# Optimization experiments

Hardware: AMD Instinct MI355X
Metric: run time of the kernel (lower is better)

Reference implementation:

```python
import jax, jax.numpy as jnp
import numpy as np

H = 2048
W = 2048

# 2x2 derivative kernels (classic Lucas-Kanade / Horn-Schunck estimates)
_KX = np.array([[-1.0, 1.0], [-1.0, 1.0]], dtype=np.float32) * 0.25
_KY = np.array([[-1.0, -1.0], [1.0, 1.0]], dtype=np.float32) * 0.25
_KT = np.array([[1.0, 1.0], [1.0, 1.0]], dtype=np.float32) * 0.25


def _conv2d(x, k, padding):
    # x: (H, W), k: (kh, kw) -> (H', W')
    return jax.lax.conv_general_dilated(
        x[None, None], k[None, None].astype(x.dtype), (1, 1), padding
    )[0, 0]


def _deriv(img, k):
    # replicate-pad bottom/right so the 2x2 valid conv returns (H, W)
    p = jnp.pad(img, ((0, 1), (0, 1)), mode='edge')
    return _conv2d(p, jnp.asarray(k), 'VALID')


def setup_inputs() -> dict:
    key = jax.random.key(0)
    k1, k2 = jax.random.split(key)
    image_prev = jax.random.uniform(k1, (1, 1, H, W), dtype=jnp.float32)
    image_next = jax.random.uniform(k2, (1, 1, H, W), dtype=jnp.float32)
    return {"image_prev": image_prev, "image_next": image_next, "window_size": 15}


def reference(image_prev, image_next, window_size):
    prev = image_prev[0, 0]  # (H, W); original code only uses batch 0, channel 0
    nxt = image_next[0, 0]

    fx = 0.5 * (_deriv(prev, _KX) + _deriv(nxt, _KX))
    fy = 0.5 * (_deriv(prev, _KY) + _deriv(nxt, _KY))
    ft = _deriv(nxt, _KT) - _deriv(prev, _KT)

    w = int(window_size)
    ones = jnp.ones((w, w), dtype=fx.dtype)

    def box(f):
        # window sum with zero padding == ZeroPad2d(n) + w x w sliding sum
        return _conv2d(f, ones, 'SAME')

    Axx = box(fx * fx)
    Axy = box(fx * fy)
    Ayy = box(fy * fy)
    bx = box(fx * ft)
    by = box(fy * ft)

    det = Axx * Ayy - Axy * Axy
    valid = det != 0
    safe_det = jnp.where(valid, det, jnp.ones_like(det))
    # [[Axx,Axy],[Axy,Ayy]]^{-1} @ [bx, by]
    u = jnp.where(valid, (Ayy * bx - Axy * by) / safe_det, 0.0)
    v = jnp.where(valid, (Axx * by - Axy * bx) / safe_det, 0.0)

    return jnp.stack([u, v])[None]  # (1, 2, H, W)
```

## Files before the change

kernel.cpp:

```cpp
#include <hip/hip_runtime.h>


constexpr int IH  = 2048;
constexpr int IW  = 2048;
constexpr int RAD = 7;
constexpr int WIN = 15;
constexpr int NT  = 256;
constexpr int SW  = 112;
constexpr int RB  = 4;
constexpr int SCAN = RB + WIN - 1;
constexpr int NSTRIP = 19;
constexpr int NBAND  = IH / RB;
constexpr int NGRP   = NBAND / 4;
constexpr int NXCD   = 8;
constexpr int CHUNK  = NGRP / NXCD;

struct Row { float sp0, sp1, dt0, dt1; };

template<bool YE>
__device__ __forceinline__ Row load_row(const float* __restrict__ P,
                                        const float* __restrict__ N,
                                        int row, int pcb, bool lload) {
    if constexpr (YE) row = row < 0 ? 0 : (row > IH - 1 ? IH - 1 : row);
    float2 q = make_float2(0.f, 0.f), r = q;
    if (lload) {
        const size_t off = (size_t)row * IW + pcb;
        q = *reinterpret_cast<const float2*>(P + off);
        r = *reinterpret_cast<const float2*>(N + off);
    }
    Row R;
    R.sp0 = q.x + r.x; R.dt0 = r.x - q.x;
    R.sp1 = q.y + r.y; R.dt1 = r.y - q.y;
    return R;
}

template<bool SUB, bool XE>
__device__ __forceinline__ void accum(float V[5][2], const Row& A, const Row& B,
                                      int t, bool ok, bool rep2) {
    const float g0 = A.sp0 + B.sp0, g1 = A.sp1 + B.sp1;
    const float m0 = B.sp0 - A.sp0, m1 = B.sp1 - A.sp1;
    const float e0 = A.dt0 + B.dt0, e1 = A.dt1 + B.dt1;
    float g2 = __shfl(g0, t + 1);
    float m2 = __shfl(m0, t + 1);
    float e2 = __shfl(e0, t + 1);
    if constexpr (XE) {
        g2 = rep2 ? g1 : g2; m2 = rep2 ? m1 : m2; e2 = rep2 ? e1 : e2;
    }
    float fx0 = g1 - g0, fy0 = m0 + m1, ft0 = e0 + e1;
    float fx1 = g2 - g1, fy1 = m1 + m2, ft1 = e1 + e2;
    if constexpr (XE) {
        fx0 = ok ? fx0 : 0.f; fy0 = ok ? fy0 : 0.f; ft0 = ok ? ft0 : 0.f;
        fx1 = ok ? fx1 : 0.f; fy1 = ok ? fy1 : 0.f; ft1 = ok ? ft1 : 0.f;
    }
    if constexpr (!SUB) {
        V[0][0] += fx0 * fx0; V[1][0] += fx0 * fy0; V[2][0] += fy0 * fy0;
        V[3][0] += fx0 * ft0; V[4][0] += fy0 * ft0;
        V[0][1] += fx1 * fx1; V[1][1] += fx1 * fy1; V[2][1] += fy1 * fy1;
        V[3][1] += fx1 * ft1; V[4][1] += fy1 * ft1;
    } else {
        V[0][0] -= fx0 * fx0; V[1][0] -= fx0 * fy0; V[2][0] -= fy0 * fy0;
        V[3][0] -= fx0 * ft0; V[4][0] -= fy0 * ft0;
        V[0][1] -= fx1 * fx1; V[1][1] -= fx1 * fy1; V[2][1] -= fy1 * fy1;
        V[3][1] -= fx1 * ft1; V[4][1] -= fy1 * ft1;
    }
}

template<bool XE, bool YE>
__device__ __forceinline__ void lk_body(const float* __restrict__ P,
                                        const float* __restrict__ N,
                                        float* __restrict__ out,
                                        int c0, int r0, int t) {
    const int pcb = c0 - 8 + 2 * t;
    bool ok = true, rep2 = false;
    if constexpr (XE) {
        ok   = ((unsigned)pcb < (unsigned)IW);
        rep2 = (pcb + 2 >= IW) && ok;
    }
    const bool lload = ok;

    float V[5][2] = {};

    Row E0 = load_row<YE>(P, N, r0 - 7, pcb, lload);
    Row E1 = load_row<YE>(P, N, r0 - 6, pcb, lload);
    Row E2 = load_row<YE>(P, N, r0 - 5, pcb, lload);
    Row X0 = E0, X1 = E1, X2 = E2, X3;

    #pragma unroll
    for (int sr = 0; sr < SCAN; ++sr) {
        const int pr = r0 - RAD + sr;

        Row nE;
        const bool doE = (sr <= 15);
        if (doE) nE = load_row<YE>(P, N, pr + 3, pcb, lload);

        bool enter_ok = true;
        if constexpr (YE) enter_ok = (pr >= 0) && (pr < IH);
        if (enter_ok) accum<false, XE>(V, E0, E1, t, ok, rep2);

        if (sr >= 15) {
            bool exit_ok = true;
            if constexpr (YE) exit_ok = (pr - WIN) >= 0;
            if (exit_ok) {
                if (sr == 15) accum<true, XE>(V, X0, X1, t, ok, rep2);
                if (sr == 16) accum<true, XE>(V, X1, X2, t, ok, rep2);
                if (sr == 17) accum<true, XE>(V, X2, X3, t, ok, rep2);
            }
        }

        if (sr >= WIN - 1) {
            float a0[5], a1[5];
            #pragma unroll
            for (int p = 0; p < 5; ++p) {
                const float Pg = V[p][0] + V[p][1];
                float S = Pg + __shfl(Pg, t + 1);
                S += __shfl(S, t + 2);
                S += __shfl(S, t + 4);
                const float q0 = __shfl(V[p][0], t + 8);
                a0[p] = S - V[p][0];
                a1[p] = (S - Pg) + q0;
            }
            const float det0 = a0[0] * a0[2] - a0[1] * a0[1];
            const float rd0  = __builtin_amdgcn_rcpf(det0) * 2.0f;
            const bool  k0   = (det0 != 0.f);
            const float det1 = a1[0] * a1[2] - a1[1] * a1[1];
            const float rd1  = __builtin_amdgcn_rcpf(det1) * 2.0f;
            const bool  k1   = (det1 != 0.f);
            float2 qu, qv;
            qu.x = k0 ? (a0[2] * a0[3] - a0[1] * a0[4]) * rd0 : 0.f;
            qv.x = k0 ? (a0[0] * a0[4] - a0[1] * a0[3]) * rd0 : 0.f;
            qu.y = k1 ? (a1[2] * a1[3] - a1[1] * a1[4]) * rd1 : 0.f;
            qv.y = k1 ? (a1[0] * a1[4] - a1[1] * a1[3]) * rd1 : 0.f;

            const int i  = r0 + sr - (WIN - 1);
            const int x0 = c0 + 2 * t;
            const bool st = (2 * t < SW) && (x0 < IW);
            if (st) {
                *reinterpret_cast<float2*>(out + (size_t)i * IW + x0) = qu;
                *reinterpret_cast<float2*>(out + (size_t)IH * IW + (size_t)i * IW + x0) = qv;
            }
        }

        E0 = E1; E1 = E2; if (doE) E2 = nE;
        if (sr == 0) X3 = nE;
    }
}

__global__ __launch_bounds__(NT)
void lk_kernel(const float* __restrict__ Pimg, const float* __restrict__ Nimg,
               float* __restrict__ out) {
    const int bid   = blockIdx.x;
    const int xcd   = bid & 7;
    const int idx   = bid >> 3;
    const int strip = idx / CHUNK;
    const int pos   = idx % CHUNK;
    const int bg    = xcd * CHUNK + pos;
    const int wid   = threadIdx.x >> 6;
    const int band  = bg * 4 + wid;
    const int t     = threadIdx.x & 63;
    const int c0 = strip * SW;
    const int r0 = band * RB;
    const bool xe = (strip == 0) || (strip == NSTRIP - 1);
    const bool ye = (band < 2) || (band >= NBAND - 2);
    if (!xe && !ye)      lk_body<false, false>(Pimg, Nimg, out, c0, r0, t);
    else if (xe && !ye)  lk_body<true,  false>(Pimg, Nimg, out, c0, r0, t);
    else if (!xe)        lk_body<false, true >(Pimg, Nimg, out, c0, r0, t);
    else                 lk_body<true,  true >(Pimg, Nimg, out, c0, r0, t);
}

extern "C" void kernel_launch(void* const* d_in, const int* in_sizes, int n_in,
                              void* d_out, int out_size, void* d_ws, size_t ws_size,
                              hipStream_t stream) {
    (void)in_sizes; (void)n_in; (void)d_ws; (void)ws_size; (void)out_size;
    const float* prev = (const float*)d_in[0];
    const float* nxt  = (const float*)d_in[1];
    float* out        = (float*)d_out;
    dim3 grid(NSTRIP * NGRP);
    dim3 block(NT);
    hipLaunchKernelGGL(lk_kernel, grid, block, 0, stream, prev, nxt, out);
}
```

Baseline: 34.64 us.

## Stage block's input rows in shared memory once and scan from LDS

Each block now cooperatively loads its 16+15 input rows of both images into LDS with float4 loads, precomputing the sum and difference planes, then the four waves scan their bands from shared memory. This removes the redundant global reloads of overlapping halo rows that each wave did independently, and it removes the YE template path by clamping rows during staging. The cost is a __syncthreads barrier and LDS occupancy. The sliding-window exit rows are now reread from LDS instead of kept in registers.

```diff
diff --git a/kernel.cpp b/kernel.cpp
--- a/kernel.cpp
+++ b/kernel.cpp
@@ -6,33 +6,21 @@
 constexpr int RAD = 7;
 constexpr int WIN = 15;
 constexpr int NT  = 256;
+constexpr int RB  = 4;
+constexpr int BR  = 4 * RB;
+constexpr int SROWS = BR + WIN;
 constexpr int SW  = 112;
-constexpr int RB  = 4;
 constexpr int SCAN = RB + WIN - 1;
 constexpr int NSTRIP = 19;
-constexpr int NBAND  = IH / RB;
-constexpr int NGRP   = NBAND / 4;
-constexpr int NXCD   = 8;
-constexpr int CHUNK  = NGRP / NXCD;
+constexpr int NGRP  = IH / BR;
+constexpr int NXCD  = 8;
+constexpr int CHUNK = NGRP / NXCD;
+
+__device__ __forceinline__ int clampi(int v, int lo, int hi) {
+    return v < lo ? lo : (v > hi ? hi : v);
+}
 
 struct Row { float sp0, sp1, dt0, dt1; };
-
-template<bool YE>
-__device__ __forceinline__ Row load_row(const float* __restrict__ P,
-                                        const float* __restrict__ N,
-                                        int row, int pcb, bool lload) {
-    if constexpr (YE) row = row < 0 ? 0 : (row > IH - 1 ? IH - 1 : row);
-    float2 q = make_float2(0.f, 0.f), r = q;
-    if (lload) {
-        const size_t off = (size_t)row * IW + pcb;
-        q = *reinterpret_cast<const float2*>(P + off);
-        r = *reinterpret_cast<const float2*>(N + off);
-    }
-    Row R;
-    R.sp0 = q.x + r.x; R.dt0 = r.x - q.x;
-    R.sp1 = q.y + r.y; R.dt1 = r.y - q.y;
-    return R;
-}
 
 template<bool SUB, bool XE>
 __device__ __forceinline__ void accum(float V[5][2], const Row& A, const Row& B,
@@ -65,47 +53,44 @@
     }
 }
 
-template<bool XE, bool YE>
-__device__ __forceinline__ void lk_body(const float* __restrict__ P,
-                                        const float* __restrict__ N,
-                                        float* __restrict__ out,
-                                        int c0, int r0, int t) {
+template<bool XE>
+__device__ __forceinline__ void scan_body(const float2* __restrict__ sp,
+                                          const float2* __restrict__ dt,
+                                          float* __restrict__ out,
+                                          int c0, int R, int wid, int t) {
+    const int r0  = R + wid * RB;
+    const int kb  = wid * RB;
     const int pcb = c0 - 8 + 2 * t;
     bool ok = true, rep2 = false;
     if constexpr (XE) {
         ok   = ((unsigned)pcb < (unsigned)IW);
         rep2 = (pcb + 2 >= IW) && ok;
     }
-    const bool lload = ok;
+
+    auto ldrow = [&](int k) -> Row {
+        const float2 a = sp[k * 64 + t];
+        const float2 b = dt[k * 64 + t];
+        Row r; r.sp0 = a.x; r.sp1 = a.y; r.dt0 = b.x; r.dt1 = b.y; return r;
+    };
 
     float V[5][2] = {};
-
-    Row E0 = load_row<YE>(P, N, r0 - 7, pcb, lload);
-    Row E1 = load_row<YE>(P, N, r0 - 6, pcb, lload);
-    Row E2 = load_row<YE>(P, N, r0 - 5, pcb, lload);
-    Row X0 = E0, X1 = E1, X2 = E2, X3;
+    Row A = ldrow(kb), B = ldrow(kb + 1), C = ldrow(kb + 2);
 
     #pragma unroll
     for (int sr = 0; sr < SCAN; ++sr) {
         const int pr = r0 - RAD + sr;
 
-        Row nE;
+        Row nC;
         const bool doE = (sr <= 15);
-        if (doE) nE = load_row<YE>(P, N, pr + 3, pcb, lload);
+        if (doE) nC = ldrow(kb + sr + 3);
+        Row XA, XB;
+        const bool doX = (sr >= WIN);
+        if (doX) { XA = ldrow(kb + sr - 15); XB = ldrow(kb + sr - 14); }
 
-        bool enter_ok = true;
-        if constexpr (YE) enter_ok = (pr >= 0) && (pr < IH);
-        if (enter_ok) accum<false, XE>(V, E0, E1, t, ok, rep2);
-
-        if (sr >= 15) {
-            bool exit_ok = true;
-            if constexpr (YE) exit_ok = (pr - WIN) >= 0;
-            if (exit_ok) {
-                if (sr == 15) accum<true, XE>(V, X0, X1, t, ok, rep2);
-                if (sr == 16) accum<true, XE>(V, X1, X2, t, ok, rep2);
-                if (sr == 17) accum<true, XE>(V, X2, X3, t, ok, rep2);
-            }
-        }
+        if (pr >= 0 && pr < IH)
+            accum<false, XE>(V, A, B, t, ok, rep2);
+        if (doX && (pr - WIN) >= 0)
+            accum<true, XE>(V, XA, XB, t, ok, rep2);
 
         if (sr >= WIN - 1) {
             float a0[5], a1[5];
@@ -133,38 +118,68 @@
 
             const int i  = r0 + sr - (WIN - 1);
             const int x0 = c0 + 2 * t;
-            const bool st = (2 * t < SW) && (x0 < IW);
-            if (st) {
+            if ((2 * t < SW) && (x0 < IW)) {
                 *reinterpret_cast<float2*>(out + (size_t)i * IW + x0) = qu;
                 *reinterpret_cast<float2*>(out + (size_t)IH * IW + (size_t)i * IW + x0) = qv;
             }
         }
 
-        E0 = E1; E1 = E2; if (doE) E2 = nE;
-        if (sr == 0) X3 = nE;
+        A = B; B = C; if (doE) C = nC;
     }
 }
 
 __global__ __launch_bounds__(NT)
 void lk_kernel(const float* __restrict__ Pimg, const float* __restrict__ Nimg,
                float* __restrict__ out) {
+    __shared__ float4 s_sp[SROWS][32];
+    __shared__ float4 s_dt[SROWS][32];
+
     const int bid   = blockIdx.x;
     const int xcd   = bid & 7;
     const int idx   = bid >> 3;
     const int strip = idx / CHUNK;
     const int pos   = idx % CHUNK;
     const int bg    = xcd * CHUNK + pos;
-    const int wid   = threadIdx.x >> 6;
-    const int band  = bg * 4 + wid;
-    const int t     = threadIdx.x & 63;
-    const int c0 = strip * SW;
-    const int r0 = band * RB;
-    const bool xe = (strip == 0) || (strip == NSTRIP - 1);
-    const bool ye = (band < 2) || (band >= NBAND - 2);
-    if (!xe && !ye)      lk_body<false, false>(Pimg, Nimg, out, c0, r0, t);
-    else if (xe && !ye)  lk_body<true,  false>(Pimg, Nimg, out, c0, r0, t);
-    else if (!xe)        lk_body<false, true >(Pimg, Nimg, out, c0, r0, t);
-    else                 lk_body<true,  true >(Pimg, Nimg, out, c0, r0, t);
+    const int c0    = strip * SW;
+    const int R     = bg * BR;
+
+    const int jq = threadIdx.x & 31;
+    const int rr = threadIdx.x >> 5;
+    const int gc = c0 - 8 + 4 * jq;
+    const bool in4 = (gc >= 0) && (gc + 3 < IW);
+    #pragma unroll
+    for (int k0 = 0; k0 < SROWS; k0 += 8) {
+        const int k = k0 + rr;
+        if (k < SROWS) {
+            const int row = clampi(R - RAD + k, 0, IH - 1);
+            const float* rp = Pimg + (size_t)row * IW;
+            const float* rn = Nimg + (size_t)row * IW;
+            float4 p, n;
+            if (in4) {
+                p = *reinterpret_cast<const float4*>(rp + gc);
+                n = *reinterpret_cast<const float4*>(rn + gc);
+            } else {
+                const int g0 = clampi(gc,     0, IW - 1);
+                const int g1 = clampi(gc + 1, 0, IW - 1);
+                const int g2 = clampi(gc + 2, 0, IW - 1);
+                const int g3 = clampi(gc + 3, 0, IW - 1);
+                p = make_float4(rp[g0], rp[g1], rp[g2], rp[g3]);
+                n = make_float4(rn[g0], rn[g1], rn[g2], rn[g3]);
+            }
+            s_sp[k][jq] = make_float4(p.x + n.x, p.y + n.y, p.z + n.z, p.w + n.w);
+            s_dt[k][jq] = make_float4(n.x - p.x, n.y - p.y, n.z - p.z, n.w - p.w);
+        }
+    }
+    __syncthreads();
+
+    const int wid = threadIdx.x >> 6;
+    const int t   = threadIdx.x & 63;
+    const float2* sp = reinterpret_cast<const float2*>(&s_sp[0][0]);
+    const float2* dt = reinterpret_cast<const float2*>(&s_dt[0][0]);
+    if (strip == 0 || strip == NSTRIP - 1)
+        scan_body<true >(sp, dt, out, c0, R, wid, t);
+    else
+        scan_body<false>(sp, dt, out, c0, R, wid, t);
 }
 
 extern "C" void kernel_launch(void* const* d_in, const int* in_sizes, int n_in,
```

Result: faster. 33.67 us (-2.8%).
